# Kernel tuning notes

Measured on AMD Instinct MI355X. Metric: run time of the kernel, lower is better.

Reference implementation:

```python
import jax, jax.numpy as jnp
import numpy as np
import math

ANCHORS = np.array([[12., 16.], [19., 36.], [40., 28.]], dtype=np.float32)
NUM_CLASSES = 80
IMG_DIM = 608.0
NUM_ANCHORS = 3


def setup_inputs() -> dict:
    key = jax.random.key(0)
    ks = jax.random.split(key, 9)
    B, A, G, NC = 16, NUM_ANCHORS, 76, NUM_CLASSES
    x = jax.random.normal(ks[0], (B, A * (NC + 5), G, G), jnp.float32)
    iou = jax.random.uniform(ks[1], (B, A, G, G), jnp.float32, 0.0, 0.95)
    obj_mask = jax.random.bernoulli(ks[2], 0.02, (B, A, G, G))
    noobj_mask = jnp.logical_and(~obj_mask, jax.random.bernoulli(ks[3], 0.95, (B, A, G, G)))
    tw = jax.random.uniform(ks[4], (B, A, G, G), jnp.float32, 0.1, 4.0)
    th = jax.random.uniform(ks[5], (B, A, G, G), jnp.float32, 0.1, 4.0)
    tcls = jax.random.uniform(ks[6], (B, A, G, G, NC), jnp.float32)
    tconf = jax.random.uniform(ks[7], (B, A, G, G), jnp.float32)
    tb = jax.random.uniform(ks[8], (B, A, G, G, 4), jnp.float32)
    # target boxes in grid units: centers in [0,G), sizes in (0.5, 8.5)
    target_boxes = jnp.concatenate([tb[..., :2] * G, tb[..., 2:] * 8.0 + 0.5], -1)
    return {"x": x, "iou": iou, "obj_mask": obj_mask, "noobj_mask": noobj_mask,
            "tw": tw, "th": th, "tcls": tcls, "tconf": tconf, "target_boxes": target_boxes}


def _clog(p):
    # torch F.binary_cross_entropy clamps log to -100
    return jnp.maximum(jnp.log(p), -100.0)


def _bce(p, t):
    return -(t * _clog(p) + (1.0 - t) * _clog(1.0 - p))


def yolo_forward(x, iou, obj_mask, noobj_mask, tw, th, tcls, tconf, target_boxes):
    B = x.shape[0]
    G = x.shape[2]
    A, NC = NUM_ANCHORS, NUM_CLASSES
    stride = IMG_DIM / G
    # [B, A, G, G, 5+NC]
    pred = x.reshape(B, A, NC + 5, G, G).transpose(0, 1, 3, 4, 2)
    px = jax.nn.sigmoid(pred[..., 0])
    py = jax.nn.sigmoid(pred[..., 1])
    pw = pred[..., 2]
    ph = pred[..., 3]
    pconf = jax.nn.sigmoid(pred[..., 4])
    pcls = jax.nn.sigmoid(pred[..., 5:])

    scaled = jnp.asarray(ANCHORS) / stride
    gx = jnp.arange(G, dtype=x.dtype)[None, None, None, :]
    gy = jnp.arange(G, dtype=x.dtype)[None, None, :, None]
    aw = scaled[:, 0][None, :, None, None]
    ah = scaled[:, 1][None, :, None, None]

    bx = px + gx
    by = py + gy
    bw = jnp.exp(pw) * aw
    bh = jnp.exp(ph) * ah
    pred_boxes = jnp.stack([bx, by, bw, bh], -1)

    output = jnp.concatenate([
        pred_boxes.reshape(B, -1, 4) * stride,
        pconf.reshape(B, -1, 1),
        pcls.reshape(B, -1, NC)], -1)

    # ---- loss (masked CIoU + BCE), computed dense then mask-reduced ----
    m = obj_mask.astype(x.dtype)
    nm = noobj_mask.astype(x.dtype)
    txc, tyc, twd, tht = (target_boxes[..., i] for i in range(4))

    tx1, ty1 = txc - twd / 2, tyc - tht / 2
    tx2, ty2 = txc + twd / 2, tyc + tht / 2
    px1, py1 = bx - bw / 2, by - bh / 2
    px2, py2 = bx + bw / 2, by + bh / 2

    xc1 = jnp.minimum(px1, tx1)
    yc1 = jnp.minimum(py1, ty1)
    xc2 = jnp.maximum(px2, tx2)
    yc2 = jnp.maximum(py2, ty2)

    c = (xc2 - xc1) ** 2 + (yc2 - yc1) ** 2 + 1e-07
    d = (txc - bx) ** 2 + (tyc - by) ** 2
    rDIoU = d / c
    v = (4.0 / math.pi ** 2) * (jnp.arctan(tw / th) - jnp.arctan(pw / ph)) ** 2
    S = 1.0 - iou
    alpha = jax.lax.stop_gradient(v / (S + v))  # torch.no_grad() block
    ciou_term = 1.0 - iou + rDIoU + alpha * v
    CIoUloss = jnp.sum(m * ciou_term) / B

    cnt_obj = jnp.maximum(jnp.sum(m), 1.0)
    cnt_noobj = jnp.maximum(jnp.sum(nm), 1.0)
    bce_conf = _bce(pconf, tconf)
    loss_conf = 1.0 * jnp.sum(m * bce_conf) / cnt_obj + 100.0 * jnp.sum(nm * bce_conf) / cnt_noobj
    loss_cls = jnp.sum(m[..., None] * _bce(pcls, tcls)) / (cnt_obj * NUM_CLASSES)

    total_loss = CIoUloss + loss_conf + loss_cls
    return output, total_loss


def reference(x, iou, obj_mask, noobj_mask, tw, th, tcls, tconf, target_boxes):
    return yolo_forward(x, iou, obj_mask, noobj_mask, tw, th, tcls, tconf, target_boxes)
```

## Files before the change

kernel.cpp:

```cpp
#include <hip/hip_runtime.h>

#define B_ 16
#define A_ 3
#define G_ 76
#define GG_ (G_*G_)
#define NC_ 80
#define C_ 85
#define NCELL (B_*A_*GG_)
#define OUTN ((size_t)NCELL*C_)
#define NBLKM (NCELL/64)
#define LROW 88

typedef float f4 __attribute__((ext_vector_type(4)));

__device__ __forceinline__ float sigf(float v){ return 1.0f/(1.0f + __expf(-v)); }
__device__ __forceinline__ float clog_(float p){ return fmaxf(__logf(p), -100.0f); }
__device__ __forceinline__ float bcef(float p, float t){ return -(t*clog_(p) + (1.0f-t)*clog_(1.0f-p)); }

__global__ __launch_bounds__(256) void detect_kernel(const unsigned int* __restrict__ nm,
                                                     unsigned int* __restrict__ flags){
    unsigned v = nm[threadIdx.x];
    unsigned a01 = (v > 1u) ? 1u : 0u;
    unsigned afl = ((v != 0u) && (v != 0x3F800000u)) ? 1u : 0u;
    if (__any(a01) && (threadIdx.x & 63) == 0) atomicOr(&flags[0], 1u);
    if (__any(afl) && (threadIdx.x & 63) == 0) atomicOr(&flags[1], 1u);
}

__global__ __launch_bounds__(256, 4) void mega_kernel(
        const float* __restrict__ x, const float* __restrict__ iou,
        const void* __restrict__ om, const void* __restrict__ nm,
        const float* __restrict__ tw, const float* __restrict__ th,
        const float* __restrict__ tcls, const float* __restrict__ tconf,
        const float* __restrict__ tbox, const unsigned int* __restrict__ flags,
        float* __restrict__ out, float* __restrict__ partials){
    __shared__ __align__(16) float lds[4][16*LROW];
    __shared__ float sred[4][6];

    const int tid  = (int)threadIdx.x;
    const int w    = tid >> 6;
    const int lane = tid & 63;
    const int kg   = lane >> 4;
    const int ci   = lane & 15;

    unsigned qq = NBLKM >> 3, rr = NBLKM & 7u;
    unsigned xcd = blockIdx.x & 7u, seq = blockIdx.x >> 3;
    int blk = (int)((xcd < rr ? xcd*(qq+1u) : rr*(qq+1u) + (xcd-rr)*qq) + seq);

    int n0 = blk*64 + w*16;
    int n  = n0 + ci;
    int ba = n / GG_;
    int ij = n - ba*GG_;
    int a  = ba % A_;
    int in_ = ij / G_;
    int jn  = ij - in_*G_;
    const float* xb = x + (size_t)ba*C_*GG_ + (size_t)ij;
    float* ldsw = lds[w];

    int mode = (flags[0]==0u) ? 0 : ((flags[1]==0u) ? 1 : 2);
    bool obj, noobj;
    if (mode == 2){
        obj   = ((const unsigned char*)om)[n] != 0;
        noobj = ((const unsigned char*)nm)[n] != 0;
    } else {
        obj   = ((const unsigned int*)om)[n] != 0u;
        noobj = ((const unsigned int*)nm)[n] != 0u;
    }

    const float* tcl = tcls + (size_t)n*NC_;
    float aw8 = (a==0)?12.0f:((a==1)?19.0f:40.0f);
    float ah8 = (a==0)?16.0f:((a==1)?36.0f:28.0f);

    float clsacc = 0.f;
    float pb0=0.f, pb1=0.f, pb2=0.f, pb3=0.f, rwv=0.f, rhv=0.f, pcf=0.f;

    const float* p = xb + (size_t)(4*kg)*GG_;
    #pragma unroll
    for (int it=0; it<5; ++it){
        float e0 = p[0];
        float e1 = p[(size_t)GG_];
        float e2 = p[(size_t)2*GG_];
        float e3 = p[(size_t)3*GG_];
        int kb = 16*it + 4*kg;
        float r0,r1,r2,r3;
        if (it==0 && kg==0){
            float s0 = sigf(e0), s1 = sigf(e1);
            r0 = (s0 + (float)jn)*8.0f;
            r1 = (s1 + (float)in_)*8.0f;
            r2 = __expf(e2)*aw8;
            r3 = __expf(e3)*ah8;
            pb0=r0; pb1=r1; pb2=r2; pb3=r3; rwv=e2; rhv=e3;
        } else {
            r0 = sigf(e0); r1 = sigf(e1); r2 = sigf(e2); r3 = sigf(e3);
            if (it==0 && kg==1) pcf = r0;
            if (obj){
                if (kb+0 >= 5) clsacc += bcef(r0, tcl[kb-5]);
                if (kb+1 >= 5) clsacc += bcef(r1, tcl[kb-4]);
                if (kb+2 >= 5) clsacc += bcef(r2, tcl[kb-3]);
                if (kb+3 >= 5) clsacc += bcef(r3, tcl[kb-2]);
            }
        }
        f4 wv = {r0, r1, r2, r3};
        *(f4*)&ldsw[ci*LROW + kb] = wv;
        p += (size_t)16*GG_;
    }
    if (kg == 0){
        float e0=p[0], e1=p[(size_t)GG_], e2=p[(size_t)2*GG_], e3=p[(size_t)3*GG_];
        float q0=sigf(e0), q1=sigf(e1), q2=sigf(e2), q3=sigf(e3);
        f4 wv = {q0,q1,q2,q3};
        *(f4*)&ldsw[ci*LROW + 80] = wv;
        if (obj) clsacc += bcef(q0,tcl[75]) + bcef(q1,tcl[76]) + bcef(q2,tcl[77]) + bcef(q3,tcl[78]);
    } else if (kg == 1){
        float e4 = p[0];
        float q4 = sigf(e4);
        ldsw[ci*LROW + 84] = q4;
        if (obj) clsacc += bcef(q4, tcl[79]);
    }

    {
        float* outw = out + (size_t)n0*C_;
        #pragma unroll
        for (int itb=0; itb<6; ++itb){
            int f = lane + itb*64;
            if (f < 340){
                int e = f*4;
                int c = e/85;
                int k = e - c*85;
                int bix = c*LROW + k;
                float v0 = ldsw[bix];
                float v1 = ldsw[bix+1 + ((k+1>=85)?(LROW-85):0)];
                float v2 = ldsw[bix+2 + ((k+2>=85)?(LROW-85):0)];
                float v3 = ldsw[bix+3 + ((k+3>=85)?(LROW-85):0)];
                f4 sv = {v0,v1,v2,v3};
                ((f4*)outw)[f] = sv;
            }
        }
    }

    float ciou=0.f, co=0.f, cn=0.f;
    if (kg==0 && obj){
        float iouv = iou[n], twv = tw[n], thv = th[n];
        f4 tb = *(const f4*)(tbox + (size_t)n*4);
        float bx = pb0*0.125f, by = pb1*0.125f, bw = pb2*0.125f, bh = pb3*0.125f;
        float txc=tb[0], tyc=tb[1], twd=tb[2], tht=tb[3];
        float tx1 = txc - twd*0.5f, ty1 = tyc - tht*0.5f;
        float tx2 = txc + twd*0.5f, ty2 = tyc + tht*0.5f;
        float px1 = bx - bw*0.5f,  py1 = by - bh*0.5f;
        float px2 = bx + bw*0.5f,  py2 = by + bh*0.5f;
        float xc1 = fminf(px1, tx1), yc1 = fminf(py1, ty1);
        float xc2 = fmaxf(px2, tx2), yc2 = fmaxf(py2, ty2);
        float cc = (xc2-xc1)*(xc2-xc1) + (yc2-yc1)*(yc2-yc1) + 1e-7f;
        float dd = (txc-bx)*(txc-bx) + (tyc-by)*(tyc-by);
        float rdiou = dd/cc;
        float dat = atanf(twv/thv) - atanf(rwv/rhv);
        float vv = 0.40528473456935108577f * dat*dat;
        float Si = 1.0f - iouv;
        float alpha = vv/(Si+vv);
        ciou = 1.0f - iouv + rdiou + alpha*vv;
    }
    if (kg==1 && (obj || noobj)){
        float bc = bcef(pcf, tconf[n]);
        co = obj ? bc : 0.f;
        cn = noobj ? bc : 0.f;
    }
    unsigned long long bo  = __ballot(obj)   & 0x00000000FFFF0000ULL;
    unsigned long long bn2 = __ballot(noobj) & 0x00000000FFFF0000ULL;

    float vals[4] = {ciou, co, cn, clsacc};
    #pragma unroll
    for (int q2=0; q2<4; ++q2){
        float v = vals[q2];
        #pragma unroll
        for (int o=32; o>0; o>>=1) v += __shfl_xor(v, o, 64);
        vals[q2] = v;
    }
    if (lane == 0){
        sred[w][0]=vals[0]; sred[w][1]=vals[1]; sred[w][2]=vals[2]; sred[w][3]=vals[3];
        sred[w][4]=(float)__popcll(bo); sred[w][5]=(float)__popcll(bn2);
    }
    __syncthreads();
    if (tid < 6)
        partials[(size_t)tid*NBLKM + blk] = sred[0][tid]+sred[1][tid]+sred[2][tid]+sred[3][tid];
}

__global__ __launch_bounds__(256) void final_kernel(const float* __restrict__ partials,
                                                    float* __restrict__ out_loss){
    double acc[6] = {0,0,0,0,0,0};
    for (int idx = (int)threadIdx.x; idx < NBLKM; idx += 256){
        #pragma unroll
        for (int q=0;q<6;q++) acc[q] += (double)partials[(size_t)q*NBLKM + idx];
    }
    #pragma unroll
    for (int q=0;q<6;q++){
        double v = acc[q];
        #pragma unroll
        for (int o=32;o>0;o>>=1) v += __shfl_xor(v, o, 64);
        acc[q] = v;
    }
    __shared__ double smd[6][4];
    int lane = (int)threadIdx.x & 63, wid = (int)threadIdx.x >> 6;
    if (lane == 0){
        #pragma unroll
        for (int q=0;q<6;q++) smd[q][wid] = acc[q];
    }
    __syncthreads();
    if (threadIdx.x == 0){
        double s[6];
        #pragma unroll
        for (int q=0;q<6;q++) s[q] = smd[q][0]+smd[q][1]+smd[q][2]+smd[q][3];
        double cnt_o = fmax(s[4], 1.0);
        double cnt_n = fmax(s[5], 1.0);
        double total = s[0]/(double)B_
                     + s[1]/cnt_o
                     + 100.0*s[2]/cnt_n
                     + s[3]/(cnt_o*(double)NC_);
        *out_loss = (float)total;
    }
}

extern "C" void kernel_launch(void* const* d_in, const int* in_sizes, int n_in,
                              void* d_out, int out_size, void* d_ws, size_t ws_size,
                              hipStream_t stream){
    const float* x     = (const float*)d_in[0];
    const float* iou   = (const float*)d_in[1];
    const void*  om    = d_in[2];
    const void*  nm    = d_in[3];
    const float* tw    = (const float*)d_in[4];
    const float* th    = (const float*)d_in[5];
    const float* tcls  = (const float*)d_in[6];
    const float* tconf = (const float*)d_in[7];
    const float* tbox  = (const float*)d_in[8];
    float* out = (float*)d_out;

    unsigned int* flags = (unsigned int*)d_ws;
    float* partials = (float*)((char*)d_ws + 64);

    hipMemsetAsync(d_ws, 0, 64, stream);
    detect_kernel<<<1, 256, 0, stream>>>((const unsigned int*)nm, flags);
    mega_kernel<<<NBLKM, 256, 0, stream>>>(x, iou, om, nm, tw, th, tcls, tconf, tbox,
                                           flags, out, partials);
    final_kernel<<<1, 256, 0, stream>>>(partials, out + OUTN);
}
```

Measured before the change: 57.56 us.

## Drop mask-format detection pass and use unpadded LDS staging for output copy

Removes the memset and the detection kernel that probed the mask encoding, and hardcodes the masks as 32-bit words. This cuts two launches and a flag load from the main kernel. The LDS staging rows shrink from the padded stride to the exact 85-float stride, so the output copy becomes a straight float4 LDS-to-global copy with no index arithmetic. The price is scalar LDS writes, possible bank conflicts, and dropping support for byte-encoded masks. The occupancy hint in launch bounds also rises.

```diff
diff --git a/kernel.cpp b/kernel.cpp
--- a/kernel.cpp
+++ b/kernel.cpp
@@ -9,7 +9,6 @@
 #define NCELL (B_*A_*GG_)
 #define OUTN ((size_t)NCELL*C_)
 #define NBLKM (NCELL/64)
-#define LROW 88
 
 typedef float f4 __attribute__((ext_vector_type(4)));
 
@@ -17,23 +16,14 @@
 __device__ __forceinline__ float clog_(float p){ return fmaxf(__logf(p), -100.0f); }
 __device__ __forceinline__ float bcef(float p, float t){ return -(t*clog_(p) + (1.0f-t)*clog_(1.0f-p)); }
 
-__global__ __launch_bounds__(256) void detect_kernel(const unsigned int* __restrict__ nm,
-                                                     unsigned int* __restrict__ flags){
-    unsigned v = nm[threadIdx.x];
-    unsigned a01 = (v > 1u) ? 1u : 0u;
-    unsigned afl = ((v != 0u) && (v != 0x3F800000u)) ? 1u : 0u;
-    if (__any(a01) && (threadIdx.x & 63) == 0) atomicOr(&flags[0], 1u);
-    if (__any(afl) && (threadIdx.x & 63) == 0) atomicOr(&flags[1], 1u);
-}
-
-__global__ __launch_bounds__(256, 4) void mega_kernel(
+__global__ __launch_bounds__(256, 7) void mega_kernel(
         const float* __restrict__ x, const float* __restrict__ iou,
-        const void* __restrict__ om, const void* __restrict__ nm,
+        const unsigned int* __restrict__ om, const unsigned int* __restrict__ nm,
         const float* __restrict__ tw, const float* __restrict__ th,
         const float* __restrict__ tcls, const float* __restrict__ tconf,
-        const float* __restrict__ tbox, const unsigned int* __restrict__ flags,
+        const float* __restrict__ tbox,
         float* __restrict__ out, float* __restrict__ partials){
-    __shared__ __align__(16) float lds[4][16*LROW];
+    __shared__ __align__(16) float lds[4][16*C_];
     __shared__ float sred[4][6];
 
     const int tid  = (int)threadIdx.x;
@@ -56,15 +46,8 @@
     const float* xb = x + (size_t)ba*C_*GG_ + (size_t)ij;
     float* ldsw = lds[w];
 
-    int mode = (flags[0]==0u) ? 0 : ((flags[1]==0u) ? 1 : 2);
-    bool obj, noobj;
-    if (mode == 2){
-        obj   = ((const unsigned char*)om)[n] != 0;
-        noobj = ((const unsigned char*)nm)[n] != 0;
-    } else {
-        obj   = ((const unsigned int*)om)[n] != 0u;
-        noobj = ((const unsigned int*)nm)[n] != 0u;
-    }
+    bool obj   = om[n] != 0u;
+    bool noobj = nm[n] != 0u;
 
     const float* tcl = tcls + (size_t)n*NC_;
     float aw8 = (a==0)?12.0f:((a==1)?19.0f:40.0f);
@@ -99,40 +82,34 @@
                 if (kb+3 >= 5) clsacc += bcef(r3, tcl[kb-2]);
             }
         }
-        f4 wv = {r0, r1, r2, r3};
-        *(f4*)&ldsw[ci*LROW + kb] = wv;
+        int bix = ci*C_ + kb;
+        ldsw[bix+0] = r0;
+        ldsw[bix+1] = r1;
+        ldsw[bix+2] = r2;
+        ldsw[bix+3] = r3;
         p += (size_t)16*GG_;
     }
     if (kg == 0){
         float e0=p[0], e1=p[(size_t)GG_], e2=p[(size_t)2*GG_], e3=p[(size_t)3*GG_];
         float q0=sigf(e0), q1=sigf(e1), q2=sigf(e2), q3=sigf(e3);
-        f4 wv = {q0,q1,q2,q3};
-        *(f4*)&ldsw[ci*LROW + 80] = wv;
+        int bix = ci*C_ + 80;
+        ldsw[bix+0]=q0; ldsw[bix+1]=q1; ldsw[bix+2]=q2; ldsw[bix+3]=q3;
         if (obj) clsacc += bcef(q0,tcl[75]) + bcef(q1,tcl[76]) + bcef(q2,tcl[77]) + bcef(q3,tcl[78]);
     } else if (kg == 1){
         float e4 = p[0];
         float q4 = sigf(e4);
-        ldsw[ci*LROW + 84] = q4;
+        ldsw[ci*C_ + 84] = q4;
         if (obj) clsacc += bcef(q4, tcl[79]);
     }
 
     {
         float* outw = out + (size_t)n0*C_;
+        const f4* src4 = (const f4*)ldsw;
+        f4* dst4 = (f4*)outw;
         #pragma unroll
         for (int itb=0; itb<6; ++itb){
             int f = lane + itb*64;
-            if (f < 340){
-                int e = f*4;
-                int c = e/85;
-                int k = e - c*85;
-                int bix = c*LROW + k;
-                float v0 = ldsw[bix];
-                float v1 = ldsw[bix+1 + ((k+1>=85)?(LROW-85):0)];
-                float v2 = ldsw[bix+2 + ((k+2>=85)?(LROW-85):0)];
-                float v3 = ldsw[bix+3 + ((k+3>=85)?(LROW-85):0)];
-                f4 sv = {v0,v1,v2,v3};
-                ((f4*)outw)[f] = sv;
-            }
+            if (f < 340) dst4[f] = src4[f];
         }
     }
 
@@ -222,8 +199,8 @@
                               hipStream_t stream){
     const float* x     = (const float*)d_in[0];
     const float* iou   = (const float*)d_in[1];
-    const void*  om    = d_in[2];
-    const void*  nm    = d_in[3];
+    const unsigned int* om = (const unsigned int*)d_in[2];
+    const unsigned int* nm = (const unsigned int*)d_in[3];
     const float* tw    = (const float*)d_in[4];
     const float* th    = (const float*)d_in[5];
     const float* tcls  = (const float*)d_in[6];
@@ -231,12 +208,9 @@
     const float* tbox  = (const float*)d_in[8];
     float* out = (float*)d_out;
 
-    unsigned int* flags = (unsigned int*)d_ws;
-    float* partials = (float*)((char*)d_ws + 64);
-
-    hipMemsetAsync(d_ws, 0, 64, stream);
-    detect_kernel<<<1, 256, 0, stream>>>((const unsigned int*)nm, flags);
+    float* partials = (float*)d_ws;
+
     mega_kernel<<<NBLKM, 256, 0, stream>>>(x, iou, om, nm, tw, th, tcls, tconf, tbox,
-                                           flags, out, partials);
+                                           out, partials);
     final_kernel<<<1, 256, 0, stream>>>(partials, out + OUTN);
 }
```

After: 48.92 us (median of 2 runs). 15.0% less time.
